# Optimization experiments

Measured on AMD Instinct MI355X. Metric: run time of the kernel, lower is better.

## Reference

```python
import jax, jax.numpy as jnp
import numpy as np

NEG_SLOPE = 0.01  # torch F.leaky_relu default

def leaky_relu(x):
    return jnp.where(x >= 0, x, NEG_SLOPE * x)

def setup_inputs() -> dict:
    key = jax.random.key(0)
    ks = jax.random.split(key, 16)
    N, D, H, L = 2048, 512, 256, 16
    # normalized-adjacency-like matrix: row sums ~0.5 to keep activations sane
    A_hat = jax.random.uniform(ks[0], (N, N), dtype=jnp.float32) / N
    X = jax.random.normal(ks[1], (N, D), dtype=jnp.float32)
    eps = jax.random.normal(ks[2], (N, L), dtype=jnp.float32)
    def lin(k, fan_out, fan_in):
        s = 1.0 / np.sqrt(fan_in)
        kw, kb = jax.random.split(k)
        W = jax.random.uniform(kw, (fan_out, fan_in), minval=-s, maxval=s, dtype=jnp.float32)
        b = jax.random.uniform(kb, (fan_out,), minval=-s, maxval=s, dtype=jnp.float32)
        return W, b
    W1, b1 = lin(ks[3], H, D)          # gcn1
    Wmu, bmu = lin(ks[4], L, H)        # gcn2_mu
    Wlv, blv = lin(ks[5], L, H)        # gcn2_logvar
    Wd1, bd1 = lin(ks[6], 2 * L, 2 * L)  # decoder_fc1
    Wd2, bd2 = lin(ks[7], 1, 2 * L)      # decoder_fc2
    return {"A_hat": A_hat, "X": X, "eps": eps,
            "W1": W1, "b1": b1, "Wmu": Wmu, "bmu": bmu,
            "Wlv": Wlv, "blv": blv, "Wd1": Wd1, "bd1": bd1,
            "Wd2": Wd2, "bd2": bd2}

def reference(A_hat, X, eps, W1, b1, Wmu, bmu, Wlv, blv, Wd1, bd1, Wd2, bd2):
    L = Wmu.shape[0]
    # --- encode: two GCN layers (A_hat @ X) @ W.T + b ---
    Hh = leaky_relu((A_hat @ X) @ W1.T + b1)           # [N, H]
    AH = A_hat @ Hh                                    # [N, H]
    mu = AH @ Wmu.T + bmu                              # [N, L]
    logvar = AH @ Wlv.T + blv                          # [N, L]
    # --- reparameterize ---
    Z = mu + eps * jnp.exp(0.5 * logvar)               # [N, L]
    # --- decode: pairwise MLP on concat(Z_i, Z_j), vectorized ---
    # fc1(concat(Zi,Zj)) = Zi @ Wd1[:, :L].T + Zj @ Wd1[:, L:].T + bd1
    P = Z @ Wd1[:, :L].T                               # [N, 2L]
    Q = Z @ Wd1[:, L:].T                               # [N, 2L]
    h = leaky_relu(P[:, None, :] + Q[None, :, :] + bd1)  # [N, N, 2L]
    A_pred = jax.nn.sigmoid(jnp.einsum('nmh,h->nm', h, Wd2[0]) + bd2[0])  # [N, N]
    return (A_pred, mu, logvar)
```

## Files before the change

### kernel.cpp

```cpp
#include <hip/hip_runtime.h>

#define NNODE 2048
#define DD    512
#define HHID  256
#define LLAT  16
#define H2    32

typedef __attribute__((ext_vector_type(8))) short  short8;
typedef __attribute__((ext_vector_type(4))) float  f32x4;

__device__ __forceinline__ unsigned short f2bf(float x) {
    unsigned int u = __float_as_uint(x);
    unsigned int r = (u + 0x7fffu + ((u >> 16) & 1u)) >> 16;
    return (unsigned short)r;
}
__device__ __forceinline__ float bf2f(unsigned short u) {
    return __uint_as_float(((unsigned int)u) << 16);
}

__global__ __launch_bounds__(256) void t0_cvt(const float* __restrict__ A,
                                              const float* __restrict__ X,
                                              const float* __restrict__ W1,
                                              unsigned short* __restrict__ Abf,
                                              unsigned short* __restrict__ Xbf,
                                              unsigned short* __restrict__ W1bf) {
    const int NT = 1343488;
    for (int v = blockIdx.x * 256 + threadIdx.x; v < NT; v += gridDim.x * 256) {
        const float* src; unsigned short* dst; int off;
        if (v < 1048576)      { src = A;  dst = Abf;  off = v; }
        else if (v < 1310720) { src = X;  dst = Xbf;  off = v - 1048576; }
        else                  { src = W1; dst = W1bf; off = v - 1310720; }
        float4 f = ((const float4*)src)[off];
        short4 h;
        h.x = (short)f2bf(f.x); h.y = (short)f2bf(f.y);
        h.z = (short)f2bf(f.z); h.w = (short)f2bf(f.w);
        ((short4*)dst)[off] = h;
    }
}

__global__ __launch_bounds__(256) void t1_mfma(const unsigned short* __restrict__ W1bf,
                                               const unsigned short* __restrict__ Xbf,
                                               float* __restrict__ XWp) {
    __shared__ __align__(16) unsigned short Ab[64][40];
    __shared__ __align__(16) unsigned short Bb[64][40];
    const int tid = threadIdx.x;
    const int n0 = blockIdx.x * 64;
    const int h0 = blockIdx.y * 64;
    const int ks = blockIdx.z;
    const int lane = tid & 63, wave = tid >> 6;
    const int wm = wave >> 1, wn = wave & 1;
    const int lm = lane & 15, lk = (lane >> 4) * 8;
    const int sr = tid >> 2, sc = (tid & 3) * 8;
    f32x4 acc[2][2] = {};
    for (int it = 0; it < 4; ++it) {
        int kk = ks * 128 + it * 32;
        *(uint4*)&Ab[sr][sc] = *(const uint4*)(W1bf + (size_t)(h0 + sr) * DD + kk + sc);
        *(uint4*)&Bb[sr][sc] = *(const uint4*)(Xbf  + (size_t)(n0 + sr) * DD + kk + sc);
        __syncthreads();
        short8 a0 = *(const short8*)&Ab[wm * 32 + lm][lk];
        short8 a1 = *(const short8*)&Ab[wm * 32 + 16 + lm][lk];
        short8 b0 = *(const short8*)&Bb[wn * 32 + lm][lk];
        short8 b1 = *(const short8*)&Bb[wn * 32 + 16 + lm][lk];
        acc[0][0] = __builtin_amdgcn_mfma_f32_16x16x32_bf16(a0, b0, acc[0][0], 0, 0, 0);
        acc[0][1] = __builtin_amdgcn_mfma_f32_16x16x32_bf16(a0, b1, acc[0][1], 0, 0, 0);
        acc[1][0] = __builtin_amdgcn_mfma_f32_16x16x32_bf16(a1, b0, acc[1][0], 0, 0, 0);
        acc[1][1] = __builtin_amdgcn_mfma_f32_16x16x32_bf16(a1, b1, acc[1][1], 0, 0, 0);
        __syncthreads();
    }
    float* outp = XWp + (size_t)ks * 524288;
    #pragma unroll
    for (int mi = 0; mi < 2; ++mi)
        #pragma unroll
        for (int ni = 0; ni < 2; ++ni)
            #pragma unroll
            for (int r = 0; r < 4; ++r) {
                int row = h0 + wm * 32 + mi * 16 + (lane >> 4) * 4 + r;
                int col = n0 + wn * 32 + ni * 16 + lm;
                outp[(size_t)row * NNODE + col] = acc[mi][ni][r];
            }
}

__global__ __launch_bounds__(256) void t1r(const float* __restrict__ XWp,
                                           unsigned short* __restrict__ XWt) {
    int v = blockIdx.x * 256 + threadIdx.x;
    const float4* p = (const float4*)XWp;
    float4 a = p[v];
    float4 b = p[v + 131072];
    float4 c = p[v + 262144];
    float4 d = p[v + 393216];
    float4 s;
    s.x = (a.x + b.x) + (c.x + d.x);
    s.y = (a.y + b.y) + (c.y + d.y);
    s.z = (a.z + b.z) + (c.z + d.z);
    s.w = (a.w + b.w) + (c.w + d.w);
    short4 h;
    h.x = (short)f2bf(s.x); h.y = (short)f2bf(s.y);
    h.z = (short)f2bf(s.z); h.w = (short)f2bf(s.w);
    ((short4*)XWt)[v] = h;
}

__global__ __launch_bounds__(256) void t2_mfma(const unsigned short* __restrict__ Abf,
                                               const unsigned short* __restrict__ XWt,
                                               float* __restrict__ Hp) {
    __shared__ __align__(16) unsigned short Ab[64][40];
    __shared__ __align__(16) unsigned short Bb[64][40];
    const int tid = threadIdx.x;
    const int m0 = blockIdx.x * 64;
    const int n0 = blockIdx.y * 64;
    const int ks = blockIdx.z;
    const int lane = tid & 63, wave = tid >> 6;
    const int wm = wave >> 1, wn = wave & 1;
    const int lm = lane & 15, lk = (lane >> 4) * 8;
    const int sr = tid >> 2, sc = (tid & 3) * 8;
    f32x4 acc[2][2] = {};
    for (int it = 0; it < 16; ++it) {
        int kk = ks * 512 + it * 32;
        *(uint4*)&Ab[sr][sc] = *(const uint4*)(Abf + (size_t)(m0 + sr) * NNODE + kk + sc);
        *(uint4*)&Bb[sr][sc] = *(const uint4*)(XWt + (size_t)(n0 + sr) * NNODE + kk + sc);
        __syncthreads();
        short8 a0 = *(const short8*)&Ab[wm * 32 + lm][lk];
        short8 a1 = *(const short8*)&Ab[wm * 32 + 16 + lm][lk];
        short8 b0 = *(const short8*)&Bb[wn * 32 + lm][lk];
        short8 b1 = *(const short8*)&Bb[wn * 32 + 16 + lm][lk];
        acc[0][0] = __builtin_amdgcn_mfma_f32_16x16x32_bf16(a0, b0, acc[0][0], 0, 0, 0);
        acc[0][1] = __builtin_amdgcn_mfma_f32_16x16x32_bf16(a0, b1, acc[0][1], 0, 0, 0);
        acc[1][0] = __builtin_amdgcn_mfma_f32_16x16x32_bf16(a1, b0, acc[1][0], 0, 0, 0);
        acc[1][1] = __builtin_amdgcn_mfma_f32_16x16x32_bf16(a1, b1, acc[1][1], 0, 0, 0);
        __syncthreads();
    }
    float* outp = Hp + (size_t)ks * 524288;
    #pragma unroll
    for (int mi = 0; mi < 2; ++mi)
        #pragma unroll
        for (int ni = 0; ni < 2; ++ni)
            #pragma unroll
            for (int r = 0; r < 4; ++r) {
                int row = m0 + wm * 32 + mi * 16 + (lane >> 4) * 4 + r;
                int col = n0 + wn * 32 + ni * 16 + lm;
                outp[(size_t)row * HHID + col] = acc[mi][ni][r];
            }
}

__global__ __launch_bounds__(256) void t2r(const float* __restrict__ Hp,
                                           const float* __restrict__ b1,
                                           unsigned short* __restrict__ Hbf) {
    int v = blockIdx.x * 256 + threadIdx.x;
    const float4* p = (const float4*)Hp;
    float4 a = p[v];
    float4 b = p[v + 131072];
    float4 c = p[v + 262144];
    float4 d = p[v + 393216];
    int dcol = (v & 63) * 4;
    float4 bb = *(const float4*)(b1 + dcol);
    float4 s;
    s.x = (a.x + b.x) + (c.x + d.x) + bb.x;
    s.y = (a.y + b.y) + (c.y + d.y) + bb.y;
    s.z = (a.z + b.z) + (c.z + d.z) + bb.z;
    s.w = (a.w + b.w) + (c.w + d.w) + bb.w;
    s.x = fmaxf(s.x, 0.01f * s.x);
    s.y = fmaxf(s.y, 0.01f * s.y);
    s.z = fmaxf(s.z, 0.01f * s.z);
    s.w = fmaxf(s.w, 0.01f * s.w);
    short4 h;
    h.x = (short)f2bf(s.x); h.y = (short)f2bf(s.y);
    h.z = (short)f2bf(s.z); h.w = (short)f2bf(s.w);
    ((short4*)Hbf)[v] = h;
}

__global__ __launch_bounds__(256) void t3_g(const unsigned short* __restrict__ Hbf,
                                            const float* __restrict__ Wmu,
                                            const float* __restrict__ Wlv,
                                            unsigned short* __restrict__ Gt) {
    __shared__ float Hs[8][260];
    __shared__ float Ws[32][260];
    const int tid = threadIdx.x;
    const int n0 = blockIdx.x * 8;
    #pragma unroll
    for (int s = 0; s < 8; ++s) {
        int idx = tid + s * 256;
        int row = idx >> 6, c = (idx & 63) * 4;
        const float* src = (row < 16) ? (Wmu + (size_t)row * HHID)
                                      : (Wlv + (size_t)(row - 16) * HHID);
        *(float4*)&Ws[row][c] = *(const float4*)(src + c);
    }
    {
        int r = tid >> 5, seg = tid & 31;
        int d = seg * 8;
        ushort4 u0 = *(const ushort4*)(Hbf + (size_t)(n0 + r) * HHID + d);
        ushort4 u1 = *(const ushort4*)(Hbf + (size_t)(n0 + r) * HHID + d + 4);
        Hs[r][d + 0] = bf2f(u0.x); Hs[r][d + 1] = bf2f(u0.y);
        Hs[r][d + 2] = bf2f(u0.z); Hs[r][d + 3] = bf2f(u0.w);
        Hs[r][d + 4] = bf2f(u1.x); Hs[r][d + 5] = bf2f(u1.y);
        Hs[r][d + 6] = bf2f(u1.z); Hs[r][d + 7] = bf2f(u1.w);
    }
    __syncthreads();
    const int r = tid >> 5, j = tid & 31;
    float acc = 0.f;
    #pragma unroll 8
    for (int d4 = 0; d4 < 64; ++d4) {
        float4 a = *(const float4*)&Hs[r][d4 * 4];
        float4 b = *(const float4*)&Ws[j][d4 * 4];
        acc += a.x * b.x + a.y * b.y + a.z * b.z + a.w * b.w;
    }
    Gt[(size_t)j * NNODE + n0 + r] = f2bf(acc);
}

__global__ __launch_bounds__(256) void t4_mfma(const unsigned short* __restrict__ Abf,
                                               const unsigned short* __restrict__ Gt,
                                               float* __restrict__ Mp) {
    __shared__ __align__(16) unsigned short Ab[64][40];
    __shared__ __align__(16) unsigned short Bb[32][40];
    const int tid = threadIdx.x;
    const int m0 = blockIdx.x * 64;
    const int ks = blockIdx.y;
    const int lane = tid & 63, wave = tid >> 6;
    const int lm = lane & 15, lk = (lane >> 4) * 8;
    const int sr = tid >> 2, sc = (tid & 3) * 8;
    f32x4 acc[2] = {};
    for (int it = 0; it < 8; ++it) {
        int kk = ks * 256 + it * 32;
        *(uint4*)&Ab[sr][sc] = *(const uint4*)(Abf + (size_t)(m0 + sr) * NNODE + kk + sc);
        if (tid < 128) {
            int row = tid >> 2, c = (tid & 3) * 8;
            *(uint4*)&Bb[row][c] = *(const uint4*)(Gt + (size_t)row * NNODE + kk + c);
        }
        __syncthreads();
        short8 a  = *(const short8*)&Ab[wave * 16 + lm][lk];
        short8 b0 = *(const short8*)&Bb[lm][lk];
        short8 b1 = *(const short8*)&Bb[16 + lm][lk];
        acc[0] = __builtin_amdgcn_mfma_f32_16x16x32_bf16(a, b0, acc[0], 0, 0, 0);
        acc[1] = __builtin_amdgcn_mfma_f32_16x16x32_bf16(a, b1, acc[1], 0, 0, 0);
        __syncthreads();
    }
    float* outp = Mp + (size_t)ks * 65536;
    #pragma unroll
    for (int ni = 0; ni < 2; ++ni)
        #pragma unroll
        for (int r = 0; r < 4; ++r) {
            int row = m0 + wave * 16 + (lane >> 4) * 4 + r;
            int col = ni * 16 + lm;
            outp[(size_t)row * H2 + col] = acc[ni][r];
        }
}

__global__ __launch_bounds__(256) void t5_z(const float* __restrict__ Mp,
                                            const float* __restrict__ bmu,
                                            const float* __restrict__ blv,
                                            const float* __restrict__ eps,
                                            const float* __restrict__ Wd1,
                                            const float* __restrict__ bd1,
                                            const float* __restrict__ Wd2,
                                            float* __restrict__ out_mu,
                                            float* __restrict__ out_lv,
                                            float* __restrict__ Pp,
                                            float* __restrict__ Qq,
                                            float* __restrict__ WP,
                                            float* __restrict__ WQ) {
    __shared__ float Zs[16][16];
    __shared__ float Psh[16][32];
    __shared__ float Qsh[16][32];
    const int tid = threadIdx.x;
    const int n0 = blockIdx.x * 16;
    {
        int nl = tid >> 4, l = tid & 15;
        int n = n0 + nl;
        float m = bmu[l], lv = blv[l];
        #pragma unroll
        for (int s = 0; s < 8; ++s) {
            m  += Mp[(size_t)s * 65536 + (size_t)n * H2 + l];
            lv += Mp[(size_t)s * 65536 + (size_t)n * H2 + 16 + l];
        }
        out_mu[(size_t)n * LLAT + l] = m;
        out_lv[(size_t)n * LLAT + l] = lv;
        Zs[nl][l] = m + eps[(size_t)n * LLAT + l] * __expf(0.5f * lv);
    }
    __syncthreads();
    #pragma unroll
    for (int p = 0; p < 2; ++p) {
        int idx = tid + p * 256;
        int nl = idx >> 5, o = idx & 31;
        int n = n0 + nl;
        float ap = bd1[o], aq = 0.f;
        #pragma unroll
        for (int l = 0; l < 16; ++l) {
            float z = Zs[nl][l];
            ap = fmaf(z, Wd1[o * H2 + l],      ap);
            aq = fmaf(z, Wd1[o * H2 + 16 + l], aq);
        }
        Pp[(size_t)n * H2 + o] = ap;
        Qq[(size_t)n * H2 + o] = aq;
        Psh[nl][o] = ap;
        Qsh[nl][o] = aq;
    }
    __syncthreads();
    if (tid < 32) {
        int nl = tid & 15, sel = tid >> 4;
        float a = 0.f;
        if (sel == 0) {
            #pragma unroll
            for (int o = 0; o < 32; ++o) a = fmaf(Wd2[o], Psh[nl][o], a);
            WP[n0 + nl] = a;
        } else {
            #pragma unroll
            for (int o = 0; o < 32; ++o) a = fmaf(Wd2[o], Qsh[nl][o], a);
            WQ[n0 + nl] = a;
        }
    }
}

__global__ __launch_bounds__(256) void t6_dec(const float* __restrict__ Pp,
                                              const float* __restrict__ Qq,
                                              const float* __restrict__ WP,
                                              const float* __restrict__ WQ,
                                              const float* __restrict__ Wd2,
                                              const float* __restrict__ bd2,
                                              float* __restrict__ Apred) {
    __shared__ float Qt[32][68];
    __shared__ float Ws2[32];
    __shared__ float WQs[64];
    const int tid = threadIdx.x;
    const int j0 = blockIdx.x * 64, i0 = blockIdx.y * 16;
    #pragma unroll
    for (int s = 0; s < 8; ++s) {
        int idx = tid + s * 256;
        int j = idx >> 5, o = idx & 31;
        Qt[o][j] = Qq[(size_t)(j0 + j) * H2 + o];
    }
    if (tid < 32) Ws2[tid] = Wd2[tid];
    if (tid >= 64 && tid < 128) WQs[tid - 64] = WQ[j0 + tid - 64];
    const int i = i0 + (tid >> 4);
    const int jq = tid & 15;
    float p[32];
    const float4* P4 = (const float4*)(Pp + (size_t)i * H2);
    #pragma unroll
    for (int c = 0; c < 8; ++c) {
        float4 v = P4[c];
        p[c * 4] = v.x; p[c * 4 + 1] = v.y; p[c * 4 + 2] = v.z; p[c * 4 + 3] = v.w;
    }
    const float WPi = WP[i];
    __syncthreads();
    f32x4 acc = {0.f, 0.f, 0.f, 0.f};
    #pragma unroll
    for (int o = 0; o < 32; ++o) {
        float4 q = *(const float4*)&Qt[o][jq * 4];
        float w = Ws2[o], po = p[o];
        acc[0] = fmaf(w, fabsf(po + q.x), acc[0]);
        acc[1] = fmaf(w, fabsf(po + q.y), acc[1]);
        acc[2] = fmaf(w, fabsf(po + q.z), acc[2]);
        acc[3] = fmaf(w, fabsf(po + q.w), acc[3]);
    }
    float4 wq = *(const float4*)&WQs[jq * 4];
    const float base = fmaf(0.505f, WPi, bd2[0]);
    float4 r;
    float l0 = fmaf(0.505f, wq.x, fmaf(0.495f, acc[0], base));
    float l1 = fmaf(0.505f, wq.y, fmaf(0.495f, acc[1], base));
    float l2 = fmaf(0.505f, wq.z, fmaf(0.495f, acc[2], base));
    float l3 = fmaf(0.505f, wq.w, fmaf(0.495f, acc[3], base));
    r.x = 1.f / (1.f + __expf(-l0));
    r.y = 1.f / (1.f + __expf(-l1));
    r.z = 1.f / (1.f + __expf(-l2));
    r.w = 1.f / (1.f + __expf(-l3));
    *(float4*)(Apred + (size_t)i * NNODE + j0 + jq * 4) = r;
}

extern "C" void kernel_launch(void* const* d_in, const int* in_sizes, int n_in,
                              void* d_out, int out_size, void* d_ws, size_t ws_size,
                              hipStream_t stream) {
    const float* A   = (const float*)d_in[0];
    const float* X   = (const float*)d_in[1];
    const float* eps = (const float*)d_in[2];
    const float* W1  = (const float*)d_in[3];
    const float* b1  = (const float*)d_in[4];
    const float* Wmu = (const float*)d_in[5];
    const float* bmu = (const float*)d_in[6];
    const float* Wlv = (const float*)d_in[7];
    const float* blv = (const float*)d_in[8];
    const float* Wd1 = (const float*)d_in[9];
    const float* bd1 = (const float*)d_in[10];
    const float* Wd2 = (const float*)d_in[11];
    const float* bd2 = (const float*)d_in[12];
    float* out = (float*)d_out;
    char* ws = (char*)d_ws;

    unsigned short* Abf  = (unsigned short*)(ws);
    unsigned short* Xbf  = (unsigned short*)(ws + 8388608);
    unsigned short* W1bf = (unsigned short*)(ws + 10485760);
    float*          XWp  = (float*)(ws + 10747904);
    unsigned short* XWt  = (unsigned short*)(ws + 19136512);
    float*          Hp   = (float*)(ws + 20185088);
    unsigned short* Hbf  = (unsigned short*)(ws + 28573696);
    unsigned short* Gt   = (unsigned short*)(ws + 29622272);
    float*          Mp   = (float*)(ws + 29753344);
    float*          Pp   = (float*)(ws + 31850496);
    float*          Qq   = (float*)(ws + 32112640);
    float*          WP   = (float*)(ws + 32374784);
    float*          WQ   = (float*)(ws + 32382976);

    float* out_mu = out + (size_t)NNODE * NNODE;
    float* out_lv = out_mu + NNODE * LLAT;

    t0_cvt <<<2048,            256, 0, stream>>>(A, X, W1, Abf, Xbf, W1bf);
    t1_mfma<<<dim3(32, 4, 4),  256, 0, stream>>>(W1bf, Xbf, XWp);
    t1r    <<<512,             256, 0, stream>>>(XWp, XWt);
    t2_mfma<<<dim3(32, 4, 4),  256, 0, stream>>>(Abf, XWt, Hp);
    t2r    <<<512,             256, 0, stream>>>(Hp, b1, Hbf);
    t3_g   <<<256,             256, 0, stream>>>(Hbf, Wmu, Wlv, Gt);
    t4_mfma<<<dim3(32, 8),     256, 0, stream>>>(Abf, Gt, Mp);
    t5_z   <<<128,             256, 0, stream>>>(Mp, bmu, blv, eps, Wd1, bd1, Wd2,
                                                 out_mu, out_lv, Pp, Qq, WP, WQ);
    t6_dec <<<dim3(32, 128),   256, 0, stream>>>(Pp, Qq, WP, WQ, Wd2, bd2, out);
}
```

Baseline: 141.2 us.

## Fuse split-K reduce into G projection and Z/P/Q computation into decoder

Merges the t2r reduction kernel into t3h, so the split-K partial sums, bias, leaky ReLU and bf16 rounding are done while staging H into shared memory. Merges t5_z into the pairwise decoder: each 64x64 tile recomputes mu, logvar, Z, P, Q and the WP/WQ dot products for its own rows and columns, instead of reading them from workspace. This removes two launches and the intermediate global round trips. In exchange the Z/P/Q work is done redundantly once per tile across 1024 blocks, and each decoder block now handles 64 rows instead of 16.

```diff
diff --git a/kernel.cpp b/kernel.cpp
--- a/kernel.cpp
+++ b/kernel.cpp
@@ -141,36 +141,11 @@
             }
 }
 
-__global__ __launch_bounds__(256) void t2r(const float* __restrict__ Hp,
+__global__ __launch_bounds__(256) void t3h(const float* __restrict__ Hp,
                                            const float* __restrict__ b1,
-                                           unsigned short* __restrict__ Hbf) {
-    int v = blockIdx.x * 256 + threadIdx.x;
-    const float4* p = (const float4*)Hp;
-    float4 a = p[v];
-    float4 b = p[v + 131072];
-    float4 c = p[v + 262144];
-    float4 d = p[v + 393216];
-    int dcol = (v & 63) * 4;
-    float4 bb = *(const float4*)(b1 + dcol);
-    float4 s;
-    s.x = (a.x + b.x) + (c.x + d.x) + bb.x;
-    s.y = (a.y + b.y) + (c.y + d.y) + bb.y;
-    s.z = (a.z + b.z) + (c.z + d.z) + bb.z;
-    s.w = (a.w + b.w) + (c.w + d.w) + bb.w;
-    s.x = fmaxf(s.x, 0.01f * s.x);
-    s.y = fmaxf(s.y, 0.01f * s.y);
-    s.z = fmaxf(s.z, 0.01f * s.z);
-    s.w = fmaxf(s.w, 0.01f * s.w);
-    short4 h;
-    h.x = (short)f2bf(s.x); h.y = (short)f2bf(s.y);
-    h.z = (short)f2bf(s.z); h.w = (short)f2bf(s.w);
-    ((short4*)Hbf)[v] = h;
-}
-
-__global__ __launch_bounds__(256) void t3_g(const unsigned short* __restrict__ Hbf,
-                                            const float* __restrict__ Wmu,
-                                            const float* __restrict__ Wlv,
-                                            unsigned short* __restrict__ Gt) {
+                                           const float* __restrict__ Wmu,
+                                           const float* __restrict__ Wlv,
+                                           unsigned short* __restrict__ Gt) {
     __shared__ float Hs[8][260];
     __shared__ float Ws[32][260];
     const int tid = threadIdx.x;
@@ -185,13 +160,29 @@
     }
     {
         int r = tid >> 5, seg = tid & 31;
-        int d = seg * 8;
-        ushort4 u0 = *(const ushort4*)(Hbf + (size_t)(n0 + r) * HHID + d);
-        ushort4 u1 = *(const ushort4*)(Hbf + (size_t)(n0 + r) * HHID + d + 4);
-        Hs[r][d + 0] = bf2f(u0.x); Hs[r][d + 1] = bf2f(u0.y);
-        Hs[r][d + 2] = bf2f(u0.z); Hs[r][d + 3] = bf2f(u0.w);
-        Hs[r][d + 4] = bf2f(u1.x); Hs[r][d + 5] = bf2f(u1.y);
-        Hs[r][d + 6] = bf2f(u1.z); Hs[r][d + 7] = bf2f(u1.w);
+        int dcol = seg * 8;
+        const float* base = Hp + (size_t)(n0 + r) * HHID + dcol;
+        #pragma unroll
+        for (int q = 0; q < 2; ++q) {
+            float4 a = *(const float4*)(base + q * 4);
+            float4 b = *(const float4*)(base + 524288 + q * 4);
+            float4 c = *(const float4*)(base + 1048576 + q * 4);
+            float4 e = *(const float4*)(base + 1572864 + q * 4);
+            float4 bb = *(const float4*)(b1 + dcol + q * 4);
+            float4 s;
+            s.x = (a.x + b.x) + (c.x + e.x) + bb.x;
+            s.y = (a.y + b.y) + (c.y + e.y) + bb.y;
+            s.z = (a.z + b.z) + (c.z + e.z) + bb.z;
+            s.w = (a.w + b.w) + (c.w + e.w) + bb.w;
+            s.x = fmaxf(s.x, 0.01f * s.x);
+            s.y = fmaxf(s.y, 0.01f * s.y);
+            s.z = fmaxf(s.z, 0.01f * s.z);
+            s.w = fmaxf(s.w, 0.01f * s.w);
+            Hs[r][dcol + q * 4 + 0] = bf2f(f2bf(s.x));
+            Hs[r][dcol + q * 4 + 1] = bf2f(f2bf(s.y));
+            Hs[r][dcol + q * 4 + 2] = bf2f(f2bf(s.z));
+            Hs[r][dcol + q * 4 + 3] = bf2f(f2bf(s.w));
+        }
     }
     __syncthreads();
     const int r = tid >> 5, j = tid & 31;
@@ -243,124 +234,110 @@
         }
 }
 
-__global__ __launch_bounds__(256) void t5_z(const float* __restrict__ Mp,
-                                            const float* __restrict__ bmu,
-                                            const float* __restrict__ blv,
-                                            const float* __restrict__ eps,
-                                            const float* __restrict__ Wd1,
-                                            const float* __restrict__ bd1,
-                                            const float* __restrict__ Wd2,
-                                            float* __restrict__ out_mu,
-                                            float* __restrict__ out_lv,
-                                            float* __restrict__ Pp,
-                                            float* __restrict__ Qq,
-                                            float* __restrict__ WP,
-                                            float* __restrict__ WQ) {
-    __shared__ float Zs[16][16];
-    __shared__ float Psh[16][32];
-    __shared__ float Qsh[16][32];
-    const int tid = threadIdx.x;
-    const int n0 = blockIdx.x * 16;
-    {
-        int nl = tid >> 4, l = tid & 15;
-        int n = n0 + nl;
+__global__ __launch_bounds__(256) void t6z(const float* __restrict__ Mp,
+                                           const float* __restrict__ bmu,
+                                           const float* __restrict__ blv,
+                                           const float* __restrict__ eps,
+                                           const float* __restrict__ Wd1,
+                                           const float* __restrict__ bd1,
+                                           const float* __restrict__ Wd2,
+                                           const float* __restrict__ bd2,
+                                           float* __restrict__ out_mu,
+                                           float* __restrict__ out_lv,
+                                           float* __restrict__ Apred) {
+    __shared__ float Zs[128][16];
+    __shared__ float Psh[64][32];
+    __shared__ float Qt[32][68];
+    __shared__ float WPs[64];
+    __shared__ float WQs[64];
+    __shared__ float Ws2[32];
+    const int tid = threadIdx.x;
+    const int j0 = blockIdx.x * 64, i0 = blockIdx.y * 64;
+    if (tid < 32) Ws2[tid] = Wd2[tid];
+    #pragma unroll
+    for (int p = 0; p < 8; ++p) {
+        int idx = tid + p * 256;
+        int nl = idx >> 4, l = idx & 15;
+        int n = (nl < 64) ? (i0 + nl) : (j0 + nl - 64);
         float m = bmu[l], lv = blv[l];
         #pragma unroll
         for (int s = 0; s < 8; ++s) {
             m  += Mp[(size_t)s * 65536 + (size_t)n * H2 + l];
             lv += Mp[(size_t)s * 65536 + (size_t)n * H2 + 16 + l];
         }
-        out_mu[(size_t)n * LLAT + l] = m;
-        out_lv[(size_t)n * LLAT + l] = lv;
+        if (blockIdx.x == 0 && nl < 64) {
+            out_mu[(size_t)n * LLAT + l] = m;
+            out_lv[(size_t)n * LLAT + l] = lv;
+        }
         Zs[nl][l] = m + eps[(size_t)n * LLAT + l] * __expf(0.5f * lv);
     }
     __syncthreads();
     #pragma unroll
-    for (int p = 0; p < 2; ++p) {
+    for (int p = 0; p < 8; ++p) {
         int idx = tid + p * 256;
         int nl = idx >> 5, o = idx & 31;
-        int n = n0 + nl;
-        float ap = bd1[o], aq = 0.f;
-        #pragma unroll
-        for (int l = 0; l < 16; ++l) {
-            float z = Zs[nl][l];
-            ap = fmaf(z, Wd1[o * H2 + l],      ap);
-            aq = fmaf(z, Wd1[o * H2 + 16 + l], aq);
-        }
-        Pp[(size_t)n * H2 + o] = ap;
-        Qq[(size_t)n * H2 + o] = aq;
+        float ap = bd1[o];
+        #pragma unroll
+        for (int l = 0; l < 16; ++l)
+            ap = fmaf(Zs[nl][l], Wd1[o * H2 + l], ap);
         Psh[nl][o] = ap;
-        Qsh[nl][o] = aq;
+    }
+    #pragma unroll
+    for (int p = 0; p < 8; ++p) {
+        int idx = tid + p * 256;
+        int jl = idx >> 5, o = idx & 31;
+        float aq = 0.f;
+        #pragma unroll
+        for (int l = 0; l < 16; ++l)
+            aq = fmaf(Zs[64 + jl][l], Wd1[o * H2 + 16 + l], aq);
+        Qt[o][jl] = aq;
     }
     __syncthreads();
-    if (tid < 32) {
-        int nl = tid & 15, sel = tid >> 4;
+    if (tid < 128) {
+        int row = tid & 63, sel = tid >> 6;
         float a = 0.f;
         if (sel == 0) {
             #pragma unroll
-            for (int o = 0; o < 32; ++o) a = fmaf(Wd2[o], Psh[nl][o], a);
-            WP[n0 + nl] = a;
+            for (int o = 0; o < 32; ++o) a = fmaf(Wd2[o], Psh[row][o], a);
+            WPs[row] = a;
         } else {
             #pragma unroll
-            for (int o = 0; o < 32; ++o) a = fmaf(Wd2[o], Qsh[nl][o], a);
-            WQ[n0 + nl] = a;
-        }
-    }
-}
-
-__global__ __launch_bounds__(256) void t6_dec(const float* __restrict__ Pp,
-                                              const float* __restrict__ Qq,
-                                              const float* __restrict__ WP,
-                                              const float* __restrict__ WQ,
-                                              const float* __restrict__ Wd2,
-                                              const float* __restrict__ bd2,
-                                              float* __restrict__ Apred) {
-    __shared__ float Qt[32][68];
-    __shared__ float Ws2[32];
-    __shared__ float WQs[64];
-    const int tid = threadIdx.x;
-    const int j0 = blockIdx.x * 64, i0 = blockIdx.y * 16;
-    #pragma unroll
-    for (int s = 0; s < 8; ++s) {
-        int idx = tid + s * 256;
-        int j = idx >> 5, o = idx & 31;
-        Qt[o][j] = Qq[(size_t)(j0 + j) * H2 + o];
-    }
-    if (tid < 32) Ws2[tid] = Wd2[tid];
-    if (tid >= 64 && tid < 128) WQs[tid - 64] = WQ[j0 + tid - 64];
-    const int i = i0 + (tid >> 4);
+            for (int o = 0; o < 32; ++o) a = fmaf(Wd2[o], Qt[o][row], a);
+            WQs[row] = a;
+        }
+    }
+    __syncthreads();
     const int jq = tid & 15;
-    float p[32];
-    const float4* P4 = (const float4*)(Pp + (size_t)i * H2);
-    #pragma unroll
-    for (int c = 0; c < 8; ++c) {
-        float4 v = P4[c];
-        p[c * 4] = v.x; p[c * 4 + 1] = v.y; p[c * 4 + 2] = v.z; p[c * 4 + 3] = v.w;
-    }
-    const float WPi = WP[i];
-    __syncthreads();
-    f32x4 acc = {0.f, 0.f, 0.f, 0.f};
-    #pragma unroll
-    for (int o = 0; o < 32; ++o) {
-        float4 q = *(const float4*)&Qt[o][jq * 4];
-        float w = Ws2[o], po = p[o];
-        acc[0] = fmaf(w, fabsf(po + q.x), acc[0]);
-        acc[1] = fmaf(w, fabsf(po + q.y), acc[1]);
-        acc[2] = fmaf(w, fabsf(po + q.z), acc[2]);
-        acc[3] = fmaf(w, fabsf(po + q.w), acc[3]);
-    }
-    float4 wq = *(const float4*)&WQs[jq * 4];
-    const float base = fmaf(0.505f, WPi, bd2[0]);
-    float4 r;
-    float l0 = fmaf(0.505f, wq.x, fmaf(0.495f, acc[0], base));
-    float l1 = fmaf(0.505f, wq.y, fmaf(0.495f, acc[1], base));
-    float l2 = fmaf(0.505f, wq.z, fmaf(0.495f, acc[2], base));
-    float l3 = fmaf(0.505f, wq.w, fmaf(0.495f, acc[3], base));
-    r.x = 1.f / (1.f + __expf(-l0));
-    r.y = 1.f / (1.f + __expf(-l1));
-    r.z = 1.f / (1.f + __expf(-l2));
-    r.w = 1.f / (1.f + __expf(-l3));
-    *(float4*)(Apred + (size_t)i * NNODE + j0 + jq * 4) = r;
+    #pragma unroll
+    for (int pass = 0; pass < 4; ++pass) {
+        const int il = pass * 16 + (tid >> 4);
+        float p[32];
+        #pragma unroll
+        for (int o = 0; o < 32; ++o) p[o] = Psh[il][o];
+        const float WPi = WPs[il];
+        f32x4 acc = {0.f, 0.f, 0.f, 0.f};
+        #pragma unroll
+        for (int o = 0; o < 32; ++o) {
+            float4 q = *(const float4*)&Qt[o][jq * 4];
+            float w = Ws2[o], po = p[o];
+            acc[0] = fmaf(w, fabsf(po + q.x), acc[0]);
+            acc[1] = fmaf(w, fabsf(po + q.y), acc[1]);
+            acc[2] = fmaf(w, fabsf(po + q.z), acc[2]);
+            acc[3] = fmaf(w, fabsf(po + q.w), acc[3]);
+        }
+        float4 wq = *(const float4*)&WQs[jq * 4];
+        const float base = fmaf(0.505f, WPi, bd2[0]);
+        float4 r;
+        float l0 = fmaf(0.505f, wq.x, fmaf(0.495f, acc[0], base));
+        float l1 = fmaf(0.505f, wq.y, fmaf(0.495f, acc[1], base));
+        float l2 = fmaf(0.505f, wq.z, fmaf(0.495f, acc[2], base));
+        float l3 = fmaf(0.505f, wq.w, fmaf(0.495f, acc[3], base));
+        r.x = 1.f / (1.f + __expf(-l0));
+        r.y = 1.f / (1.f + __expf(-l1));
+        r.z = 1.f / (1.f + __expf(-l2));
+        r.w = 1.f / (1.f + __expf(-l3));
+        *(float4*)(Apred + (size_t)(i0 + il) * NNODE + j0 + jq * 4) = r;
+    }
 }
 
 extern "C" void kernel_launch(void* const* d_in, const int* in_sizes, int n_in,
@@ -388,13 +365,8 @@
     float*          XWp  = (float*)(ws + 10747904);
     unsigned short* XWt  = (unsigned short*)(ws + 19136512);
     float*          Hp   = (float*)(ws + 20185088);
-    unsigned short* Hbf  = (unsigned short*)(ws + 28573696);
-    unsigned short* Gt   = (unsigned short*)(ws + 29622272);
-    float*          Mp   = (float*)(ws + 29753344);
-    float*          Pp   = (float*)(ws + 31850496);
-    float*          Qq   = (float*)(ws + 32112640);
-    float*          WP   = (float*)(ws + 32374784);
-    float*          WQ   = (float*)(ws + 32382976);
+    unsigned short* Gt   = (unsigned short*)(ws + 28573696);
+    float*          Mp   = (float*)(ws + 28704768);
 
     float* out_mu = out + (size_t)NNODE * NNODE;
     float* out_lv = out_mu + NNODE * LLAT;
@@ -403,10 +375,8 @@
     t1_mfma<<<dim3(32, 4, 4),  256, 0, stream>>>(W1bf, Xbf, XWp);
     t1r    <<<512,             256, 0, stream>>>(XWp, XWt);
     t2_mfma<<<dim3(32, 4, 4),  256, 0, stream>>>(Abf, XWt, Hp);
-    t2r    <<<512,             256, 0, stream>>>(Hp, b1, Hbf);
-    t3_g   <<<256,             256, 0, stream>>>(Hbf, Wmu, Wlv, Gt);
+    t3h    <<<256,             256, 0, stream>>>(Hp, b1, Wmu, Wlv, Gt);
     t4_mfma<<<dim3(32, 8),     256, 0, stream>>>(Abf, Gt, Mp);
-    t5_z   <<<128,             256, 0, stream>>>(Mp, bmu, blv, eps, Wd1, bd1, Wd2,
-                                                 out_mu, out_lv, Pp, Qq, WP, WQ);
-    t6_dec <<<dim3(32, 128),   256, 0, stream>>>(Pp, Qq, WP, WQ, Wd2, bd2, out);
-}
+    t6z    <<<dim3(32, 32),    256, 0, stream>>>(Mp, bmu, blv, eps, Wd1, bd1,
+                                                 Wd2, bd2, out_mu, out_lv, out);
+}
```

Measured after the change: 195.7 us. +38.6%, slower.
